# Performance work log

Hardware: AMD Instinct MI355X
Metric: run time of the kernel (lower is better)

## Reference

```python
import jax, jax.numpy as jnp
import numpy as np

B, D1, D2, H = 8, 5, 6, 128
C = D1 * D2            # cross_band_num = 30
L = H * H              # 16384, flattened adjacency per sample
NCLASSES = 5
LIMIT = int(0.5 * L)   # limit_num = attention_lim * num_inputs = 8192
ECA_K = 3              # int(abs((log2(30)+1)/2)) = 2 -> even -> 3
ATT_K = 13             # kernel_size=12 -> even -> 13


def conv1d(x, w):
    # x: (B, 1, L), w: (1, 1, K); PyTorch Conv1d is cross-correlation, same as lax conv
    pad = w.shape[-1] // 2
    return jax.lax.conv_general_dilated(x, w, (1,), [(pad, pad)],
                                        dimension_numbers=('NCH', 'OIH', 'NCH'))


def setup_inputs() -> dict:
    key = jax.random.key(0)
    ks = jax.random.split(key, 9)
    s = lambda k, shape, scale: jax.random.normal(k, shape, jnp.float32) * scale
    return {
        'adj': jax.random.normal(ks[0], (B, D1, D2, H, H), jnp.float32),
        'eca_w': s(ks[1], (1, 1, ECA_K), 0.5),
        'att_w': s(ks[2], (1, 1, ATT_K), 0.2),
        'W1': s(ks[3], (6000, L), 0.01),
        'b1': s(ks[4], (6000,), 0.01),
        'W2': s(ks[5], (4914, 6000), 0.01),
        'b2': s(ks[6], (4914,), 0.01),
        'Wc1': s(ks[7], (32, 4914), 0.02),
        'Wc2': s(ks[8], (NCLASSES, 32), 0.1),
    }


def reference(adj, eca_w, att_w, W1, b1, W2, b2, Wc1, Wc2):
    # Vectorized over the original per-sample Python loop. Dropout omitted (eval mode).
    x = adj.reshape(B, C, H, H)
    # --- ECA channel attention ---
    pooled = x.mean(axis=(2, 3))                                   # (B, C) adaptive avg pool
    scale = jax.nn.sigmoid(conv1d(pooled[:, None, :], eca_w))[:, 0, :]  # (B, C)
    band_score = scale
    y = (x * scale[:, :, None, None]).sum(axis=1)                  # (B, H, H)
    # --- data_normal: per-sample min-max normalize ---
    mn = y.min(axis=(1, 2), keepdims=True)
    mx = y.max(axis=(1, 2), keepdims=True)
    y = (y - mn) / (mx - mn)
    v = y.reshape(B, L)
    # --- connect_attention2 (kernel 13): conv score + sigmoid + top-k scatter ---
    score = jax.nn.sigmoid(conv1d(v[:, None, :], att_w))[:, 0, :]  # (B, L)
    vals, idx = jax.lax.top_k(score, LIMIT)                        # keep largest LIMIT scores
    kept = jnp.take_along_axis(v, idx, axis=1) * (vals + 1.0)
    sparse = jnp.zeros_like(v).at[jnp.arange(B)[:, None], idx].set(kept)
    # --- dense encoder + classifier ---
    h = sparse @ W1.T + b1
    h = h @ W2.T + b2
    logits = (h @ Wc1.T) @ Wc2.T                                   # (B, NCLASSES)
    out = jax.nn.log_softmax(logits, axis=-1)
    return out, band_score
```

## Files before the change

### kernel.cpp

```cpp
#include <hip/hip_runtime.h>
#include <math.h>

#define NB 8
#define NCH 30
#define LL 16384
#define N1 6000
#define N2 4914
#define NCLS 5
#define KLIM 8192
#define ATT_K 13

typedef float f32x4 __attribute__((ext_vector_type(4)));

__device__ __forceinline__ unsigned fkey(float f) {
  unsigned u = __float_as_uint(f);
  unsigned m = (unsigned)(((int)u) >> 31) | 0x80000000u;
  return u ^ m;
}
__device__ __forceinline__ float sigmoidf(float x) { return 1.f / (1.f + expf(-x)); }

__global__ void k_pool(const float* __restrict__ adj, float* __restrict__ pooled) {
  int bc = blockIdx.x;
  const float* p = adj + (size_t)bc * LL;
  int tid = threadIdx.x;
  float s = 0.f;
  #pragma unroll
  for (int it = 0; it < LL / (256 * 4); ++it) {
    float4 v = *(const float4*)(p + it * 1024 + tid * 4);
    s += v.x + v.y + v.z + v.w;
  }
  #pragma unroll
  for (int m = 1; m < 64; m <<= 1) s += __shfl_xor(s, m);
  __shared__ float red[4];
  if ((tid & 63) == 0) red[tid >> 6] = s;
  __syncthreads();
  if (tid == 0) pooled[bc] = (red[0] + red[1] + red[2] + red[3]) * (1.f / (float)LL);
}

__global__ void k_wsum(const float* __restrict__ adj, const float* __restrict__ pooled,
                       const float* __restrict__ ew, float* __restrict__ y,
                       float* __restrict__ pmm, float* __restrict__ band_out) {
  int blk = blockIdx.x;
  int b = blk >> 4, tile = blk & 15;
  int tid = threadIdx.x;
  __shared__ float sc[NCH];
  if (tid < NCH) {
    int c = tid;
    const float* p = pooled + b * NCH;
    float s = ew[1] * p[c];
    if (c > 0)       s += ew[0] * p[c - 1];
    if (c < NCH - 1) s += ew[2] * p[c + 1];
    float scv = sigmoidf(s);
    sc[c] = scv;
    if (tile == 0) band_out[b * NCH + c] = scv;
  }
  __syncthreads();
  int j = tile * 1024 + tid * 4;
  const float* base = adj + (size_t)b * NCH * LL + j;
  float4 acc = {0.f, 0.f, 0.f, 0.f};
  #pragma unroll
  for (int c = 0; c < NCH; ++c) {
    float4 v = *(const float4*)(base + (size_t)c * LL);
    float s = sc[c];
    acc.x += v.x * s; acc.y += v.y * s; acc.z += v.z * s; acc.w += v.w * s;
  }
  *(float4*)(y + b * LL + j) = acc;
  float mn = fminf(fminf(acc.x, acc.y), fminf(acc.z, acc.w));
  float mx = fmaxf(fmaxf(acc.x, acc.y), fmaxf(acc.z, acc.w));
  #pragma unroll
  for (int m = 1; m < 64; m <<= 1) {
    mn = fminf(mn, __shfl_xor(mn, m));
    mx = fmaxf(mx, __shfl_xor(mx, m));
  }
  __shared__ float wmn[4], wmx[4];
  if ((tid & 63) == 0) { wmn[tid >> 6] = mn; wmx[tid >> 6] = mx; }
  __syncthreads();
  if (tid == 0) {
    mn = fminf(fminf(wmn[0], wmn[1]), fminf(wmn[2], wmn[3]));
    mx = fmaxf(fmaxf(wmx[0], wmx[1]), fmaxf(wmx[2], wmx[3]));
    pmm[blk * 2 + 0] = mn; pmm[blk * 2 + 1] = mx;
  }
}

__global__ __launch_bounds__(1024) void k_selfuse(const float* __restrict__ y,
                                                  const float* __restrict__ pmm,
                                                  const float* __restrict__ w,
                                                  float* __restrict__ sp) {
  int b = blockIdx.x;
  int tid = threadIdx.x;
  int wave = tid >> 6, lane = tid & 63;
  extern __shared__ float vsh[];
  __shared__ float wl[ATT_K];
  __shared__ int redw[16][3];
  __shared__ int ctot[3];
  __shared__ int wtot[16];
  if (tid < ATT_K) wl[tid] = w[tid];

  float mn = pmm[b * 32], mx = pmm[b * 32 + 1];
  #pragma unroll
  for (int t = 1; t < 16; ++t) {
    mn = fminf(mn, pmm[b * 32 + t * 2]);
    mx = fmaxf(mx, pmm[b * 32 + t * 2 + 1]);
  }
  float inv = 1.f / (mx - mn);

  const float* yb = y + b * LL;
  #pragma unroll
  for (int c = 0; c < 4; ++c) {
    int i = c * 4096 + tid * 4;
    float4 t4 = *(const float4*)(yb + i);
    int p0 = i + (i >> 5);
    vsh[p0 + 0] = (t4.x - mn) * inv;
    vsh[p0 + 1] = (t4.y - mn) * inv;
    vsh[p0 + 2] = (t4.z - mn) * inv;
    vsh[p0 + 3] = (t4.w - mn) * inv;
  }
  __syncthreads();

  int e = tid * 16;
  unsigned kk[16];
  {
    float v28[28];
    #pragma unroll
    for (int i = 0; i < 28; ++i) {
      int j = e - 6 + i;
      v28[i] = (j >= 0 && j < LL) ? vsh[j + (j >> 5)] : 0.f;
    }
    #pragma unroll
    for (int i = 0; i < 16; ++i) {
      float acc = 0.f;
      #pragma unroll
      for (int k = 0; k < ATT_K; ++k) acc += v28[i + k] * wl[k];
      kk[i] = fkey(acc);
    }
  }

  unsigned p = 0; int need = KLIM;
  for (int pass = 0; pass < 16; ++pass) {
    int sh = 30 - pass * 2;
    unsigned himask = (pass == 0) ? 0u : (0xFFFFFFFFu << (sh + 2));
    int c3 = 0, c2 = 0, c1 = 0;
    #pragma unroll
    for (int i = 0; i < 16; ++i) {
      unsigned k2 = kk[i];
      if ((k2 & himask) == p) {
        unsigned bk = (k2 >> sh) & 3u;
        c3 += (bk == 3); c2 += (bk == 2); c1 += (bk == 1);
      }
    }
    #pragma unroll
    for (int m = 1; m < 64; m <<= 1) {
      c3 += __shfl_xor(c3, m); c2 += __shfl_xor(c2, m); c1 += __shfl_xor(c1, m);
    }
    if (lane == 0) { redw[wave][0] = c3; redw[wave][1] = c2; redw[wave][2] = c1; }
    __syncthreads();
    if (wave == 0) {
      int a0 = 0, a1 = 0, a2 = 0;
      if (lane < 16) { a0 = redw[lane][0]; a1 = redw[lane][1]; a2 = redw[lane][2]; }
      #pragma unroll
      for (int m = 1; m < 16; m <<= 1) {
        a0 += __shfl_xor(a0, m); a1 += __shfl_xor(a1, m); a2 += __shfl_xor(a2, m);
      }
      if (lane == 0) { ctot[0] = a0; ctot[1] = a1; ctot[2] = a2; }
    }
    __syncthreads();
    int C3 = ctot[0], C2 = ctot[1], C1 = ctot[2];
    if (C3 >= need)                { p |= 3u << sh; }
    else if (C3 + C2 >= need)      { p |= 2u << sh; need -= C3; }
    else if (C3 + C2 + C1 >= need) { p |= 1u << sh; need -= C3 + C2; }
    else                           { need -= C3 + C2 + C1; }
  }

  int cnt = 0;
  #pragma unroll
  for (int i = 0; i < 16; ++i) cnt += (kk[i] == p);
  int pre = cnt;
  #pragma unroll
  for (int m = 1; m < 64; m <<= 1) {
    int t = __shfl_up(pre, m);
    if (lane >= m) pre += t;
  }
  if (lane == 63) wtot[wave] = pre;
  __syncthreads();
  int base = 0;
  for (int t = 0; t < 16; ++t) if (t < wave) base += wtot[t];
  int rank = base + pre - cnt;

  float v28[28];
  #pragma unroll
  for (int i = 0; i < 28; ++i) {
    int j = e - 6 + i;
    v28[i] = (j >= 0 && j < LL) ? vsh[j + (j >> 5)] : 0.f;
  }
  float outv[16];
  #pragma unroll
  for (int i = 0; i < 16; ++i) {
    float acc = 0.f;
    #pragma unroll
    for (int k = 0; k < ATT_K; ++k) acc += v28[i + k] * wl[k];
    bool sel;
    if (kk[i] > p) sel = true;
    else if (kk[i] == p) { sel = (rank < need); rank++; }
    else sel = false;
    outv[i] = sel ? v28[i + 6] * (sigmoidf(acc) + 1.f) : 0.f;
  }
  float* spb = sp + b * LL + e;
  #pragma unroll
  for (int q = 0; q < 4; ++q)
    *(f32x4*)(spb + q * 4) = *(f32x4*)(outv + q * 4);
}

__global__ __launch_bounds__(1024, 4) void k_gemm1(const float* __restrict__ W1,
                                                   const float* __restrict__ sp,
                                                   float* __restrict__ p1) {
  __shared__ float sps[8][2048];
  int bid = blockIdx.x;
  int s = bid & 7, g = bid >> 3;
  int tid = threadIdx.x, wave = tid >> 6, lane = tid & 63;
  #pragma unroll
  for (int i = 0; i < 4; ++i) {
    int idx = i * 1024 + tid;
    int bb = idx >> 9, off = (idx & 511) * 4;
    *(f32x4*)&sps[bb][off] = *(const f32x4*)(sp + (size_t)bb * LL + s * 2048 + off);
  }
  __syncthreads();
  int r0 = g * 94;
  int nr = N1 - r0; if (nr > 94) nr = 94;
  int npair = nr >> 1;
  for (int p = wave; p < npair; p += 16) {
    int rA = r0 + p * 2;
    const float* wpA = W1 + (size_t)rA * LL + s * 2048;
    const float* wpB = wpA + LL;
    float acc0[8], acc1[8];
    #pragma unroll
    for (int bb = 0; bb < 8; ++bb) { acc0[bb] = 0.f; acc1[bb] = 0.f; }
    #pragma unroll 2
    for (int it = 0; it < 8; ++it) {
      int k0 = it * 256 + lane * 4;
      f32x4 wA = __builtin_nontemporal_load((const f32x4*)(wpA + k0));
      f32x4 wB = __builtin_nontemporal_load((const f32x4*)(wpB + k0));
      #pragma unroll
      for (int bb = 0; bb < 8; ++bb) {
        f32x4 s4 = *(const f32x4*)&sps[bb][k0];
        acc0[bb] += wA.x * s4.x + wA.y * s4.y + wA.z * s4.z + wA.w * s4.w;
        acc1[bb] += wB.x * s4.x + wB.y * s4.y + wB.z * s4.z + wB.w * s4.w;
      }
    }
    #pragma unroll
    for (int bb = 0; bb < 8; ++bb) {
      float a0 = acc0[bb], a1 = acc1[bb];
      #pragma unroll
      for (int m = 1; m < 64; m <<= 1) {
        a0 += __shfl_xor(a0, m);
        a1 += __shfl_xor(a1, m);
      }
      if (lane == 0) {
        p1[(size_t)(s * 8 + bb) * N1 + rA]     = a0;
        p1[(size_t)(s * 8 + bb) * N1 + rA + 1] = a1;
      }
    }
  }
}

__global__ __launch_bounds__(1024, 4) void k_gemm2(const float* __restrict__ W2,
                                                   const float* __restrict__ p1,
                                                   const float* __restrict__ b1,
                                                   float* __restrict__ p2) {
  __shared__ float hs[8][2048];
  int bid = blockIdx.x;
  int s = bid / 86, g = bid % 86;
  int ks = s * 2048;
  int klen = (s == 2) ? (N1 - 4096) : 2048;
  int tid = threadIdx.x, wave = tid >> 6, lane = tid & 63;
  #pragma unroll
  for (int i = 0; i < 4; ++i) {
    int idx = i * 1024 + tid;
    int bb = idx >> 9, off = (idx & 511) * 4;
    f32x4 v = {0.f, 0.f, 0.f, 0.f};
    if (off < klen) {
      int j = ks + off;
      #pragma unroll
      for (int q = 0; q < 8; ++q)
        v += *(const f32x4*)(p1 + (size_t)(q * 8 + bb) * N1 + j);
      v += *(const f32x4*)(b1 + j);
    }
    *(f32x4*)&hs[bb][off] = v;
  }
  __syncthreads();
  int r0 = g * 58;
  int nr = N2 - r0; if (nr > 58) nr = 58; if (nr < 0) nr = 0;
  int npair = nr >> 1;
  for (int p = wave; p < npair; p += 16) {
    int rA = r0 + p * 2;
    const float* wpA = W2 + (size_t)rA * N1 + ks;
    const float* wpB = wpA + N1;
    float acc0[8], acc1[8];
    #pragma unroll
    for (int bb = 0; bb < 8; ++bb) { acc0[bb] = 0.f; acc1[bb] = 0.f; }
    #pragma unroll 2
    for (int it = 0; it < 8; ++it) {
      int k0 = it * 256 + lane * 4;
      f32x4 wA = __builtin_nontemporal_load((const f32x4*)(wpA + k0));
      f32x4 wB = __builtin_nontemporal_load((const f32x4*)(wpB + k0));
      #pragma unroll
      for (int bb = 0; bb < 8; ++bb) {
        f32x4 s4 = *(const f32x4*)&hs[bb][k0];
        acc0[bb] += wA.x * s4.x + wA.y * s4.y + wA.z * s4.z + wA.w * s4.w;
        acc1[bb] += wB.x * s4.x + wB.y * s4.y + wB.z * s4.z + wB.w * s4.w;
      }
    }
    #pragma unroll
    for (int bb = 0; bb < 8; ++bb) {
      float a0 = acc0[bb], a1 = acc1[bb];
      #pragma unroll
      for (int m = 1; m < 64; m <<= 1) {
        a0 += __shfl_xor(a0, m);
        a1 += __shfl_xor(a1, m);
      }
      if (lane == 0) {
        p2[(size_t)(s * 8 + bb) * N2 + rA]     = a0;
        p2[(size_t)(s * 8 + bb) * N2 + rA + 1] = a1;
      }
    }
  }
}

__global__ void k_cls1(const float* __restrict__ p2, const float* __restrict__ b2,
                       const float* __restrict__ Wc1, float* __restrict__ t) {
  int bid = blockIdx.x; int b = bid >> 5, m = bid & 31;
  int tid = threadIdx.x;
  const float* wm = Wc1 + m * N2;
  float s = 0.f;
  for (int j = tid; j < N2; j += 256) {
    float hv = p2[(size_t)(0 * 8 + b) * N2 + j]
             + p2[(size_t)(1 * 8 + b) * N2 + j]
             + p2[(size_t)(2 * 8 + b) * N2 + j] + b2[j];
    s += hv * wm[j];
  }
  #pragma unroll
  for (int mm = 1; mm < 64; mm <<= 1) s += __shfl_xor(s, mm);
  __shared__ float red[4];
  if ((tid & 63) == 0) red[tid >> 6] = s;
  __syncthreads();
  if (tid == 0) t[b * 32 + m] = red[0] + red[1] + red[2] + red[3];
}

__global__ void k_final(const float* __restrict__ t, const float* __restrict__ Wc2,
                        float* __restrict__ out) {
  int b = threadIdx.x;
  if (b < NB) {
    float lg[NCLS];
    #pragma unroll
    for (int k = 0; k < NCLS; ++k) {
      float s = 0.f;
      #pragma unroll
      for (int m = 0; m < 32; ++m) s += t[b * 32 + m] * Wc2[k * 32 + m];
      lg[k] = s;
    }
    float mx = lg[0];
    #pragma unroll
    for (int k = 1; k < NCLS; ++k) mx = fmaxf(mx, lg[k]);
    float se = 0.f;
    #pragma unroll
    for (int k = 0; k < NCLS; ++k) se += expf(lg[k] - mx);
    float lse = logf(se);
    #pragma unroll
    for (int k = 0; k < NCLS; ++k) out[b * NCLS + k] = lg[k] - mx - lse;
  }
}

extern "C" void kernel_launch(void* const* d_in, const int* in_sizes, int n_in,
                              void* d_out, int out_size, void* d_ws, size_t ws_size,
                              hipStream_t stream) {
  const float* adj   = (const float*)d_in[0];
  const float* eca_w = (const float*)d_in[1];
  const float* att_w = (const float*)d_in[2];
  const float* W1    = (const float*)d_in[3];
  const float* b1    = (const float*)d_in[4];
  const float* W2    = (const float*)d_in[5];
  const float* b2    = (const float*)d_in[6];
  const float* Wc1   = (const float*)d_in[7];
  const float* Wc2   = (const float*)d_in[8];
  float* out = (float*)d_out;
  float* ws  = (float*)d_ws;

  float* pooled = ws;
  float* pmm    = ws + 512;
  float* tbuf   = ws + 768;
  float* y      = ws + 1024;
  float* sp     = y  + NB * LL;
  float* p1     = sp + NB * LL;
  float* p2     = p1 + 384000;

  k_pool   <<<NB * NCH, 256, 0, stream>>>(adj, pooled);
  k_wsum   <<<NB * 16, 256, 0, stream>>>(adj, pooled, eca_w, y, pmm, out + NB * NCLS);
  k_selfuse<<<NB, 1024, 16896 * sizeof(float), stream>>>(y, pmm, att_w, sp);
  k_gemm1  <<<8 * 64, 1024, 0, stream>>>(W1, sp, p1);
  k_gemm2  <<<3 * 86, 1024, 0, stream>>>(W2, p1, b1, p2);
  k_cls1   <<<NB * 32, 256, 0, stream>>>(p2, b2, Wc1, tbuf);
  k_final  <<<1, 64, 0, stream>>>(tbuf, Wc2, out);
}
```

Baseline: 180.4 us.

## Fuse classifier tail kernels, halve radix-select syncs, retile weighted sum

Merges the two classifier kernels into a single per-sample kernel that computes Wc1 and Wc2 and the log-softmax, dropping one launch and the intermediate buffer. The radix-select loop now uses double-buffered shared counts, and every wave does the 16-entry cross-wave reduction itself, so each pass needs one barrier instead of two. k_wsum uses 256 blocks of 128 threads to spread the 30-channel reduction over more CUs, and the W2 loads in gemm2 are bounds-guarded. The tail kernel runs only 8 blocks, so the Wc1 reduction has less parallelism than before.

```diff
diff --git a/kernel.cpp b/kernel.cpp
--- a/kernel.cpp
+++ b/kernel.cpp
@@ -37,11 +37,12 @@
   if (tid == 0) pooled[bc] = (red[0] + red[1] + red[2] + red[3]) * (1.f / (float)LL);
 }
 
-__global__ void k_wsum(const float* __restrict__ adj, const float* __restrict__ pooled,
-                       const float* __restrict__ ew, float* __restrict__ y,
-                       float* __restrict__ pmm, float* __restrict__ band_out) {
+__global__ __launch_bounds__(128) void k_wsum(const float* __restrict__ adj,
+                                              const float* __restrict__ pooled,
+                                              const float* __restrict__ ew, float* __restrict__ y,
+                                              float* __restrict__ pmm, float* __restrict__ band_out) {
   int blk = blockIdx.x;
-  int b = blk >> 4, tile = blk & 15;
+  int b = blk >> 5, tile = blk & 31;
   int tid = threadIdx.x;
   __shared__ float sc[NCH];
   if (tid < NCH) {
@@ -55,7 +56,7 @@
     if (tile == 0) band_out[b * NCH + c] = scv;
   }
   __syncthreads();
-  int j = tile * 1024 + tid * 4;
+  int j = tile * 512 + tid * 4;
   const float* base = adj + (size_t)b * NCH * LL + j;
   float4 acc = {0.f, 0.f, 0.f, 0.f};
   #pragma unroll
@@ -72,13 +73,12 @@
     mn = fminf(mn, __shfl_xor(mn, m));
     mx = fmaxf(mx, __shfl_xor(mx, m));
   }
-  __shared__ float wmn[4], wmx[4];
+  __shared__ float wmn[2], wmx[2];
   if ((tid & 63) == 0) { wmn[tid >> 6] = mn; wmx[tid >> 6] = mx; }
   __syncthreads();
   if (tid == 0) {
-    mn = fminf(fminf(wmn[0], wmn[1]), fminf(wmn[2], wmn[3]));
-    mx = fmaxf(fmaxf(wmx[0], wmx[1]), fmaxf(wmx[2], wmx[3]));
-    pmm[blk * 2 + 0] = mn; pmm[blk * 2 + 1] = mx;
+    pmm[blk * 2 + 0] = fminf(wmn[0], wmn[1]);
+    pmm[blk * 2 + 1] = fmaxf(wmx[0], wmx[1]);
   }
 }
 
@@ -91,16 +91,15 @@
   int wave = tid >> 6, lane = tid & 63;
   extern __shared__ float vsh[];
   __shared__ float wl[ATT_K];
-  __shared__ int redw[16][3];
-  __shared__ int ctot[3];
+  __shared__ int redw[2][16][3];
   __shared__ int wtot[16];
   if (tid < ATT_K) wl[tid] = w[tid];
 
-  float mn = pmm[b * 32], mx = pmm[b * 32 + 1];
-  #pragma unroll
-  for (int t = 1; t < 16; ++t) {
-    mn = fminf(mn, pmm[b * 32 + t * 2]);
-    mx = fmaxf(mx, pmm[b * 32 + t * 2 + 1]);
+  float mn = pmm[b * 64], mx = pmm[b * 64 + 1];
+  #pragma unroll
+  for (int t = 1; t < 32; ++t) {
+    mn = fminf(mn, pmm[b * 64 + t * 2]);
+    mx = fmaxf(mx, pmm[b * 64 + t * 2 + 1]);
   }
   float inv = 1.f / (mx - mn);
 
@@ -139,6 +138,7 @@
   for (int pass = 0; pass < 16; ++pass) {
     int sh = 30 - pass * 2;
     unsigned himask = (pass == 0) ? 0u : (0xFFFFFFFFu << (sh + 2));
+    int buf = pass & 1;
     int c3 = 0, c2 = 0, c1 = 0;
     #pragma unroll
     for (int i = 0; i < 16; ++i) {
@@ -152,19 +152,15 @@
     for (int m = 1; m < 64; m <<= 1) {
       c3 += __shfl_xor(c3, m); c2 += __shfl_xor(c2, m); c1 += __shfl_xor(c1, m);
     }
-    if (lane == 0) { redw[wave][0] = c3; redw[wave][1] = c2; redw[wave][2] = c1; }
+    if (lane == 0) { redw[buf][wave][0] = c3; redw[buf][wave][1] = c2; redw[buf][wave][2] = c1; }
     __syncthreads();
-    if (wave == 0) {
-      int a0 = 0, a1 = 0, a2 = 0;
-      if (lane < 16) { a0 = redw[lane][0]; a1 = redw[lane][1]; a2 = redw[lane][2]; }
-      #pragma unroll
-      for (int m = 1; m < 16; m <<= 1) {
-        a0 += __shfl_xor(a0, m); a1 += __shfl_xor(a1, m); a2 += __shfl_xor(a2, m);
-      }
-      if (lane == 0) { ctot[0] = a0; ctot[1] = a1; ctot[2] = a2; }
-    }
-    __syncthreads();
-    int C3 = ctot[0], C2 = ctot[1], C1 = ctot[2];
+    int a0 = 0, a1 = 0, a2 = 0;
+    if (lane < 16) { a0 = redw[buf][lane][0]; a1 = redw[buf][lane][1]; a2 = redw[buf][lane][2]; }
+    #pragma unroll
+    for (int m = 1; m < 16; m <<= 1) {
+      a0 += __shfl_xor(a0, m); a1 += __shfl_xor(a1, m); a2 += __shfl_xor(a2, m);
+    }
+    int C3 = __shfl(a0, 0), C2 = __shfl(a1, 0), C1 = __shfl(a2, 0);
     if (C3 >= need)                { p |= 3u << sh; }
     else if (C3 + C2 >= need)      { p |= 2u << sh; need -= C3; }
     else if (C3 + C2 + C1 >= need) { p |= 1u << sh; need -= C3 + C2; }
@@ -290,6 +286,7 @@
   int r0 = g * 58;
   int nr = N2 - r0; if (nr > 58) nr = 58; if (nr < 0) nr = 0;
   int npair = nr >> 1;
+  f32x4 z = {0.f, 0.f, 0.f, 0.f};
   for (int p = wave; p < npair; p += 16) {
     int rA = r0 + p * 2;
     const float* wpA = W2 + (size_t)rA * N1 + ks;
@@ -300,8 +297,9 @@
     #pragma unroll 2
     for (int it = 0; it < 8; ++it) {
       int k0 = it * 256 + lane * 4;
-      f32x4 wA = __builtin_nontemporal_load((const f32x4*)(wpA + k0));
-      f32x4 wB = __builtin_nontemporal_load((const f32x4*)(wpB + k0));
+      bool inb = k0 < klen;
+      f32x4 wA = inb ? __builtin_nontemporal_load((const f32x4*)(wpA + k0)) : z;
+      f32x4 wB = inb ? __builtin_nontemporal_load((const f32x4*)(wpB + k0)) : z;
       #pragma unroll
       for (int bb = 0; bb < 8; ++bb) {
         f32x4 s4 = *(const f32x4*)&hs[bb][k0];
@@ -325,36 +323,37 @@
   }
 }
 
-__global__ void k_cls1(const float* __restrict__ p2, const float* __restrict__ b2,
-                       const float* __restrict__ Wc1, float* __restrict__ t) {
-  int bid = blockIdx.x; int b = bid >> 5, m = bid & 31;
+__global__ __launch_bounds__(1024) void k_tail(const float* __restrict__ p2,
+                                               const float* __restrict__ b2,
+                                               const float* __restrict__ Wc1,
+                                               const float* __restrict__ Wc2,
+                                               float* __restrict__ out) {
+  int b = blockIdx.x;
   int tid = threadIdx.x;
-  const float* wm = Wc1 + m * N2;
-  float s = 0.f;
-  for (int j = tid; j < N2; j += 256) {
-    float hv = p2[(size_t)(0 * 8 + b) * N2 + j]
-             + p2[(size_t)(1 * 8 + b) * N2 + j]
-             + p2[(size_t)(2 * 8 + b) * N2 + j] + b2[j];
-    s += hv * wm[j];
-  }
-  #pragma unroll
-  for (int mm = 1; mm < 64; mm <<= 1) s += __shfl_xor(s, mm);
-  __shared__ float red[4];
-  if ((tid & 63) == 0) red[tid >> 6] = s;
-  __syncthreads();
-  if (tid == 0) t[b * 32 + m] = red[0] + red[1] + red[2] + red[3];
-}
-
-__global__ void k_final(const float* __restrict__ t, const float* __restrict__ Wc2,
-                        float* __restrict__ out) {
-  int b = threadIdx.x;
-  if (b < NB) {
+  int wave = tid >> 6, lane = tid & 63;
+  __shared__ float tt[32];
+  const float* pb0 = p2 + (size_t)(0 * 8 + b) * N2;
+  const float* pb1 = p2 + (size_t)(1 * 8 + b) * N2;
+  const float* pb2 = p2 + (size_t)(2 * 8 + b) * N2;
+  for (int m = wave; m < 32; m += 16) {
+    const float* wm = Wc1 + m * N2;
+    float s = 0.f;
+    for (int j = lane; j < N2; j += 64) {
+      float hv = pb0[j] + pb1[j] + pb2[j] + b2[j];
+      s += hv * wm[j];
+    }
+    #pragma unroll
+    for (int mm = 1; mm < 64; mm <<= 1) s += __shfl_xor(s, mm);
+    if (lane == 0) tt[m] = s;
+  }
+  __syncthreads();
+  if (tid == 0) {
     float lg[NCLS];
     #pragma unroll
     for (int k = 0; k < NCLS; ++k) {
       float s = 0.f;
       #pragma unroll
-      for (int m = 0; m < 32; ++m) s += t[b * 32 + m] * Wc2[k * 32 + m];
+      for (int m = 0; m < 32; ++m) s += tt[m] * Wc2[k * 32 + m];
       lg[k] = s;
     }
     float mx = lg[0];
@@ -385,18 +384,16 @@
   float* ws  = (float*)d_ws;
 
   float* pooled = ws;
-  float* pmm    = ws + 512;
-  float* tbuf   = ws + 768;
+  float* pmm    = ws + 256;
   float* y      = ws + 1024;
   float* sp     = y  + NB * LL;
   float* p1     = sp + NB * LL;
   float* p2     = p1 + 384000;
 
   k_pool   <<<NB * NCH, 256, 0, stream>>>(adj, pooled);
-  k_wsum   <<<NB * 16, 256, 0, stream>>>(adj, pooled, eca_w, y, pmm, out + NB * NCLS);
+  k_wsum   <<<NB * 32, 128, 0, stream>>>(adj, pooled, eca_w, y, pmm, out + NB * NCLS);
   k_selfuse<<<NB, 1024, 16896 * sizeof(float), stream>>>(y, pmm, att_w, sp);
   k_gemm1  <<<8 * 64, 1024, 0, stream>>>(W1, sp, p1);
   k_gemm2  <<<3 * 86, 1024, 0, stream>>>(W2, p1, b1, p2);
-  k_cls1   <<<NB * 32, 256, 0, stream>>>(p2, b2, Wc1, tbuf);
-  k_final  <<<1, 64, 0, stream>>>(tbuf, Wc2, out);
-}
+  k_tail   <<<NB, 1024, 0, stream>>>(p2, b2, Wc1, Wc2, out);
+}
```

After: 240.9 us. +33.5%, slower.
